# Optimization experiments

Measured on AMD Instinct MI355X. Metric: run time of the kernel, lower is better.

## Reference

```python
import jax, jax.numpy as jnp
import numpy as np
from jax import lax


def setup_inputs() -> dict:
    key = jax.random.key(0)
    x = jax.random.normal(key, (4, 8192, 3), dtype=jnp.float32)
    return {"x": x, "k": 16}


def reference(x, k):
    p = x[..., :3]                                  # (B, N, 3)
    # Brute-force KNN: squared euclidean distances (B, N, N)
    sq = jnp.sum(p * p, axis=-1)                    # (B, N)
    d2 = sq[:, :, None] + sq[:, None, :] - 2.0 * jnp.einsum('bnd,bmd->bnm', p, p)
    _, idx = lax.top_k(-d2, k)                      # (B, N, k), nearest (incl. self)
    # Gather neighbors per batch
    neighbors = jax.vmap(lambda pts, ids: pts[ids])(p, idx)   # (B, N, k, 3)
    mean = jnp.mean(neighbors, axis=2, keepdims=True)          # (B, N, 1, 3)
    diff = neighbors - mean                                    # (B, N, k, 3)
    # cov = mean_k (diff diff^T) over neighbors -> (B, N, 3, 3)
    cov = jnp.einsum('bnki,bnkj->bnij', diff, diff) / k
    ev = jnp.linalg.eigvalsh(cov)                  # ascending: (B, N, 3)
    lambda0 = ev[..., 2]
    lambda1 = ev[..., 1]
    return lambda0 / lambda1
```

## Files before the change

### kernel.cpp

```cpp
#include <hip/hip_runtime.h>
#include <math.h>

#define NB 4
#define NP 8192
#define KK 16
#define QPB 64
#define NPTS (NB * NP)

#define TSAMP 2048
#define TTCH 256
#define BCH 1024
#define NBCH 8
#define CAP 30
#define SROW 34
#define SCH (64 * SROW + 2)
#define K32Q 137
#define J16Q 130
#define PADKEY 0xFFFFFFFFFFFFull
#define TAU_MARGIN 2.5e-4f

#define CSWAP_DESC(a, b) { float _lo = fminf(a, b); float _hi = fmaxf(a, b); a = _hi; b = _lo; }
#define CSWAP_ASC(a, b)  { float _lo = fminf(a, b); float _hi = fmaxf(a, b); a = _lo; b = _hi; }

__device__ __forceinline__ float ref_sq(float x, float y, float z) {
  return __fadd_rn(__fadd_rn(__fmul_rn(x, x), __fmul_rn(y, y)), __fmul_rn(z, z));
}

__device__ __forceinline__ float ref_d2(float qx, float qy, float qz, float sqq,
                                        float cx, float cy, float cz) {
  float sqc = ref_sq(cx, cy, cz);
  float dot = __fadd_rn(__fadd_rn(__fmul_rn(qx, cx), __fmul_rn(qy, cy)),
                        __fmul_rn(qz, cz));
  float s = __fadd_rn(sqq, sqc);
  return __fmaf_rn(-2.0f, dot, s);
}

__device__ __forceinline__ float diff_d2(float qx, float qy, float qz,
                                         float cx, float cy, float cz) {
  float dx = cx - qx, dy = cy - qy, dz = cz - qz;
  return __fmaf_rn(dz, dz, __fmaf_rn(dy, dy, dx * dx));
}

__device__ __forceinline__ unsigned int ord_f32(float d) {
  unsigned int b = __float_as_uint(d);
  return b ^ ((b >> 31) ? 0xFFFFFFFFu : 0x80000000u);
}

__device__ __forceinline__ double eigen_ratio_tail(
    float cxx, float cyy, float czz, float cxy, float cxz, float cyz,
    float k1) {
  double a   = (double)__fmul_rn(cxx, k1), b = (double)__fmul_rn(cyy, k1);
  double c2  = (double)__fmul_rn(czz, k1);
  double dxy = (double)__fmul_rn(cxy, k1), exz = (double)__fmul_rn(cxz, k1);
  double fyz = (double)__fmul_rn(cyz, k1);
  double qm = (a + b + c2) / 3.0;
  double p1 = dxy * dxy + exz * exz + fyz * fyz;
  double aa = a - qm, bb = b - qm, cc = c2 - qm;
  double p2 = aa * aa + bb * bb + cc * cc + 2.0 * p1;
  if (p2 <= 0.0) return 1.0;
  double p  = sqrt(p2 / 6.0);
  double ip = 1.0 / p;
  double b00 = aa * ip, b11 = bb * ip, b22 = cc * ip;
  double b01 = dxy * ip, b02 = exz * ip, b12 = fyz * ip;
  double detB = b00 * (b11 * b22 - b12 * b12)
              - b01 * (b01 * b22 - b12 * b02)
              + b02 * (b01 * b12 - b11 * b02);
  double r = 0.5 * detB;
  r = fmin(1.0, fmax(-1.0, r));
  const double dcl = 2.0 * r;
  float phif = acosf((float)r) * (1.0f / 3.0f);
  double y0 = 2.0 * (double)cosf(phif);
  double y2 = 2.0 * (double)cosf(phif + 2.0943951f);
#pragma unroll
  for (int it = 0; it < 3; ++it) {
    double g0 = 3.0 * (y0 * y0 - 1.0);
    if (fabs(g0) > 1e-4) y0 -= (y0 * y0 * y0 - 3.0 * y0 - dcl) / g0;
    double g2 = 3.0 * (y2 * y2 - 1.0);
    if (fabs(g2) > 1e-4) y2 -= (y2 * y2 * y2 - 3.0 * y2 - dcl) / g2;
  }
  double e0 = qm + p * y0;
  double e2v = qm + p * y2;
  double e1 = 3.0 * qm - e0 - e2v;
  return e0 / e1;
}

__device__ __forceinline__ void topk_update(float bd[KK], float d[8]) {
  CSWAP_DESC(d[0], d[1]) CSWAP_DESC(d[2], d[3]) CSWAP_DESC(d[4], d[5]) CSWAP_DESC(d[6], d[7])
  CSWAP_DESC(d[0], d[2]) CSWAP_DESC(d[1], d[3]) CSWAP_DESC(d[4], d[6]) CSWAP_DESC(d[5], d[7])
  CSWAP_DESC(d[1], d[2]) CSWAP_DESC(d[5], d[6])
  CSWAP_DESC(d[0], d[4]) CSWAP_DESC(d[1], d[5]) CSWAP_DESC(d[2], d[6]) CSWAP_DESC(d[3], d[7])
  CSWAP_DESC(d[2], d[4]) CSWAP_DESC(d[3], d[5])
  CSWAP_DESC(d[1], d[2]) CSWAP_DESC(d[3], d[4]) CSWAP_DESC(d[5], d[6])
#pragma unroll
  for (int i = 0; i < 8; ++i) bd[8 + i] = fminf(bd[8 + i], d[i]);
#pragma unroll
  for (int i = 0; i < 8; ++i)  CSWAP_ASC(bd[i], bd[i + 8])
#pragma unroll
  for (int i = 0; i < 4; ++i)  CSWAP_ASC(bd[i], bd[i + 4])
#pragma unroll
  for (int i = 8; i < 12; ++i) CSWAP_ASC(bd[i], bd[i + 4])
#pragma unroll
  for (int g = 0; g < 4; ++g) {
    CSWAP_ASC(bd[4 * g + 0], bd[4 * g + 2]) CSWAP_ASC(bd[4 * g + 1], bd[4 * g + 3])
    CSWAP_ASC(bd[4 * g + 0], bd[4 * g + 1]) CSWAP_ASC(bd[4 * g + 2], bd[4 * g + 3])
  }
}

__global__ __launch_bounds__(512, 4) void filter_select_kernel(
    const float* __restrict__ x, float* __restrict__ out) {
  extern __shared__ __align__(16) char smem[];
  float4* samp = (float4*)smem;
  float (*s_t)[64][17] = (float (*)[64][17])smem;
  unsigned short* s_idx = (unsigned short*)smem;
  unsigned int* k32 = (unsigned int*)smem;
  unsigned short* j16s = (unsigned short*)(smem + 35072);
  unsigned short* s_cnt = (unsigned short*)(smem + 51712);
  float* s_tau = (float*)(smem + 52736);

  const int tid   = threadIdx.x;
  const int lane  = tid & 63;
  const int w     = __builtin_amdgcn_readfirstlane(tid >> 6);
  const int group = blockIdx.x;
  const int batch = group >> 7;
  const int qbase = (group & 127) * QPB;
  const float* __restrict__ Xb = x + (size_t)batch * NP * 3;

  const float qx = Xb[3 * (qbase + lane) + 0];
  const float qy = Xb[3 * (qbase + lane) + 1];
  const float qz = Xb[3 * (qbase + lane) + 2];

  {
    const float4* X4 = (const float4*)Xb;
#pragma unroll
    for (int r = 0; r < 3; ++r)
      samp[r * 512 + tid] = X4[r * 512 + tid];
  }
  __syncthreads();

  float bdA[KK], bdB[KK];
  {
    const float* sf = (const float*)samp;
#pragma unroll
    for (int t = 0; t < KK; ++t) { bdA[t] = 3.4e38f; bdB[t] = 3.4e38f; }

    const int j0 = w * TTCH;
    for (int jj = 0; jj < TTCH; jj += 16) {
      float dA[8], dB[8];
#pragma unroll
      for (int u = 0; u < 8; ++u) {
        const int j = 3 * (j0 + jj + u);
        dA[u] = diff_d2(qx, qy, qz, sf[j], sf[j + 1], sf[j + 2]);
      }
#pragma unroll
      for (int u = 0; u < 8; ++u) {
        const int j = 3 * (j0 + jj + 8 + u);
        dB[u] = diff_d2(qx, qy, qz, sf[j], sf[j + 1], sf[j + 2]);
      }
      topk_update(bdA, dA);
      topk_update(bdB, dB);
    }
    topk_update(bdA, &bdB[0]);
    topk_update(bdA, &bdB[8]);
  }
  __syncthreads();

#pragma unroll
  for (int t = 0; t < KK; ++t) s_t[w][lane][t] = bdA[t];
  __syncthreads();

  if (w == 0) {
    float md[KK];
#pragma unroll
    for (int t = 0; t < KK; ++t) md[t] = s_t[0][lane][t];
#pragma unroll
    for (int s2 = 1; s2 < NBCH; ++s2) {
      float d[KK];
#pragma unroll
      for (int t = 0; t < KK; ++t) d[t] = s_t[s2][lane][t];
      topk_update(md, &d[0]);
      topk_update(md, &d[8]);
    }
    s_tau[lane] = md[KK - 1];
  }
  __syncthreads();

  {
    const int j0 = w * BCH;
    const float tau = s_tau[lane] + TAU_MARGIN;
    unsigned short* Srow = &s_idx[w * SCH + lane * SROW];
    int cnt = 0;
    for (int jj = 0; jj < BCH; jj += 16) {
      const float4* xp = (const float4*)(Xb + (size_t)(j0 + jj) * 3);
      float4 cv[12];
#pragma unroll
      for (int u = 0; u < 12; ++u) cv[u] = xp[u];
      const float* f = (const float*)cv;
#pragma unroll
      for (int u = 0; u < 16; ++u) {
        float d = diff_d2(qx, qy, qz, f[3 * u], f[3 * u + 1], f[3 * u + 2]);
        if (d <= tau) {
          if (cnt < CAP) Srow[1 + cnt] = (unsigned short)(j0 + jj + u);
          ++cnt;
        }
      }
    }
    s_cnt[w * 64 + lane] = (unsigned short)cnt;
  }
  __syncthreads();

  const int qlq = tid >> 3;
  const int pch = tid & 7;
  unsigned long long slots[KK];
#pragma unroll
  for (int t = 0; t < KK; ++t) slots[t] = PADKEY;
  {
    const float q2x = Xb[3 * (qbase + qlq) + 0];
    const float q2y = Xb[3 * (qbase + qlq) + 1];
    const float q2z = Xb[3 * (qbase + qlq) + 2];
    const float sq2 = ref_sq(q2x, q2y, q2z);
    const unsigned short* row = &s_idx[pch * SCH + qlq * SROW + 1];
    int cnl = (int)s_cnt[pch * 64 + qlq];
    if (cnl > CAP) cnl = CAP;
    for (int e = 0; e < cnl; e += 8) {
      unsigned long long kv[8];
#pragma unroll
      for (int u = 0; u < 8; ++u) {
        const bool ok = (e + u) < cnl;
        const int j = ok ? (int)row[e + u] : 0;
        const float cx = Xb[3 * j], cy = Xb[3 * j + 1], cz = Xb[3 * j + 2];
        const float dd = ref_d2(q2x, q2y, q2z, sq2, cx, cy, cz);
        kv[u] = ok ? ((((unsigned long long)ord_f32(dd)) << 16) |
                      (unsigned int)j)
                   : PADKEY;
      }
#pragma unroll
      for (int u = 0; u < 8; ++u) {
        const unsigned long long k = kv[u];
        if (k < slots[KK - 1]) {
#pragma unroll
          for (int t = KK - 1; t >= 1; --t) {
            unsigned long long lo =
                (slots[t] < k) ? slots[t] : k;
            slots[t] = (slots[t - 1] > lo) ? slots[t - 1] : lo;
          }
          slots[0] = (slots[0] < k) ? slots[0] : k;
        }
      }
    }
  }
  __syncthreads();

#pragma unroll
  for (int t = 0; t < KK; ++t) {
    k32[qlq * K32Q + pch * 17 + t] = (unsigned int)(slots[t] >> 16);
    j16s[qlq * J16Q + pch * 16 + t] = (unsigned short)(slots[t] & 0xFFFFull);
  }
  __syncthreads();

  if (tid < QPB) {
    const int ql = tid;
    const int qg = batch * NP + qbase + ql;
    const float q2x = Xb[3 * (qbase + ql) + 0];
    const float q2y = Xb[3 * (qbase + ql) + 1];
    const float q2z = Xb[3 * (qbase + ql) + 2];
    const float sq2 = ref_sq(q2x, q2y, q2z);

    int total = 0;
    bool fs = false;
#pragma unroll
    for (int p = 0; p < NBCH; ++p) {
      const int c = (int)s_cnt[p * 64 + ql];
      if (c > CAP) fs = true;
      total += c;
    }
    if (total < KK) fs = true;

    int mjr[KK];
    if (!fs) {
      const unsigned int* kq = k32 + ql * K32Q;
      const unsigned short* jq = j16s + ql * J16Q;
      int head[NBCH];
#pragma unroll
      for (int p = 0; p < NBCH; ++p) head[p] = 0;
#pragma unroll
      for (int t = 0; t < KK; ++t) {
        unsigned long long best = PADKEY;
        int bp = 0;
#pragma unroll
        for (int p = 0; p < NBCH; ++p) {
          const int h = head[p];
          const unsigned long long k =
              (h < KK) ? ((((unsigned long long)kq[p * 17 + h]) << 16) |
                          jq[p * 16 + h])
                       : PADKEY;
          if (k < best) { best = k; bp = p; }
        }
        head[bp]++;
        mjr[t] = (int)(best & 0xFFFFull);
      }
    } else {
      float md[KK];
#pragma unroll
      for (int t = 0; t < KK; ++t) { md[t] = 3.4e38f; mjr[t] = 0; }
      for (int j = 0; j < NP; ++j) {
        float d = ref_d2(q2x, q2y, q2z, sq2,
                         Xb[3 * j], Xb[3 * j + 1], Xb[3 * j + 2]);
        if (d < md[KK - 1]) {
          bool c0 = d < md[0];
#pragma unroll
          for (int t = KK - 1; t >= 1; --t) {
            bool cl = d < md[t];
            bool cp = d < md[t - 1];
            float nv = fmaxf(md[t - 1], fminf(md[t], d));
            mjr[t] = cl ? (cp ? mjr[t - 1] : j) : mjr[t];
            md[t] = nv;
          }
          mjr[0] = c0 ? j : mjr[0];
          md[0] = fminf(md[0], d);
        }
      }
    }

    float px[KK], py[KK], pz[KK];
#pragma unroll
    for (int s = 0; s < KK; ++s) {
      px[s] = Xb[3 * mjr[s]];
      py[s] = Xb[3 * mjr[s] + 1];
      pz[s] = Xb[3 * mjr[s] + 2];
    }

    float sx = 0.f, sy = 0.f, sz = 0.f;
#pragma unroll
    for (int s = 0; s < KK; ++s) {
      sx = __fadd_rn(sx, px[s]);
      sy = __fadd_rn(sy, py[s]);
      sz = __fadd_rn(sz, pz[s]);
    }
    const float k1 = 1.0f / KK;
    const float mx = sx * k1, my = sy * k1, mz = sz * k1;

    float cxx = 0.f, cxy = 0.f, cxz = 0.f, cyy = 0.f, cyz = 0.f, czz = 0.f;
#pragma unroll
    for (int s = 0; s < KK; ++s) {
      float dx = __fsub_rn(px[s], mx);
      float dy = __fsub_rn(py[s], my);
      float dz = __fsub_rn(pz[s], mz);
      cxx = __fadd_rn(cxx, __fmul_rn(dx, dx));
      cxy = __fadd_rn(cxy, __fmul_rn(dx, dy));
      cxz = __fadd_rn(cxz, __fmul_rn(dx, dz));
      cyy = __fadd_rn(cyy, __fmul_rn(dy, dy));
      cyz = __fadd_rn(cyz, __fmul_rn(dy, dz));
      czz = __fadd_rn(czz, __fmul_rn(dz, dz));
    }

    out[qg] = (float)eigen_ratio_tail(cxx, cyy, czz, cxy, cxz, cyz, k1);
  }
}

extern "C" void kernel_launch(void* const* d_in, const int* in_sizes, int n_in,
                              void* d_out, int out_size, void* d_ws, size_t ws_size,
                              hipStream_t stream) {
  const float* x = (const float*)d_in[0];
  float* out = (float*)d_out;
  const size_t fs_lds = 52992;
  filter_select_kernel<<<dim3(512), dim3(512), fs_lds, stream>>>(x, out);
}
```

Measured before the change: 185.5 us.

## Merge per-chunk top-k lists via wavefront shuffles and bitonic merge; branchless candidate append

Drops the two barriers and the LDS staging of each chunk's sorted 16-slot keys. The eight lanes serving a query now merge their lists in registers using xor-shuffles and a bitonic half-cleaner network, so the single-thread 8-way merge per query goes away. The candidate filter loop now writes unconditionally to a clamped slot and increments the count branchlessly, which avoids lane divergence. LDS use drops from about 53 KB to 36 KB, which may allow more blocks per CU. The cost is 48 64-bit shuffles per lane and more register pressure.

```diff
diff --git a/kernel.cpp b/kernel.cpp
--- a/kernel.cpp
+++ b/kernel.cpp
@@ -14,13 +14,13 @@
 #define CAP 30
 #define SROW 34
 #define SCH (64 * SROW + 2)
-#define K32Q 137
-#define J16Q 130
 #define PADKEY 0xFFFFFFFFFFFFull
 #define TAU_MARGIN 2.5e-4f
 
 #define CSWAP_DESC(a, b) { float _lo = fminf(a, b); float _hi = fmaxf(a, b); a = _hi; b = _lo; }
 #define CSWAP_ASC(a, b)  { float _lo = fminf(a, b); float _hi = fmaxf(a, b); a = _lo; b = _hi; }
+#define CSWAP_U64(a, b)  { unsigned long long _lo = (a < b) ? a : b; \
+                           unsigned long long _hi = (a < b) ? b : a; a = _lo; b = _hi; }
 
 __device__ __forceinline__ float ref_sq(float x, float y, float z) {
   return __fadd_rn(__fadd_rn(__fmul_rn(x, x), __fmul_rn(y, y)), __fmul_rn(z, z));
@@ -112,10 +112,8 @@
   float4* samp = (float4*)smem;
   float (*s_t)[64][17] = (float (*)[64][17])smem;
   unsigned short* s_idx = (unsigned short*)smem;
-  unsigned int* k32 = (unsigned int*)smem;
-  unsigned short* j16s = (unsigned short*)(smem + 35072);
-  unsigned short* s_cnt = (unsigned short*)(smem + 51712);
-  float* s_tau = (float*)(smem + 52736);
+  unsigned short* s_cnt = (unsigned short*)(smem + 34848);
+  float* s_tau = (float*)(smem + 35872);
 
   const int tid   = threadIdx.x;
   const int lane  = tid & 63;
@@ -197,11 +195,10 @@
       const float* f = (const float*)cv;
 #pragma unroll
       for (int u = 0; u < 16; ++u) {
-        float d = diff_d2(qx, qy, qz, f[3 * u], f[3 * u + 1], f[3 * u + 2]);
-        if (d <= tau) {
-          if (cnt < CAP) Srow[1 + cnt] = (unsigned short)(j0 + jj + u);
-          ++cnt;
-        }
+        const float d = diff_d2(qx, qy, qz, f[3 * u], f[3 * u + 1], f[3 * u + 2]);
+        const int wofs = (cnt < CAP) ? cnt : CAP;
+        Srow[1 + wofs] = (unsigned short)(j0 + jj + u);
+        cnt += (d <= tau) ? 1 : 0;
       }
     }
     s_cnt[w * 64 + lane] = (unsigned short)cnt;
@@ -248,17 +245,35 @@
       }
     }
   }
-  __syncthreads();
-
-#pragma unroll
-  for (int t = 0; t < KK; ++t) {
-    k32[qlq * K32Q + pch * 17 + t] = (unsigned int)(slots[t] >> 16);
-    j16s[qlq * J16Q + pch * 16 + t] = (unsigned short)(slots[t] & 0xFFFFull);
-  }
-  __syncthreads();
-
-  if (tid < QPB) {
-    const int ql = tid;
+
+#pragma unroll
+  for (int m = 1; m <= 4; m <<= 1) {
+    unsigned long long pr[KK];
+#pragma unroll
+    for (int t = 0; t < KK; ++t)
+      pr[t] = (unsigned long long)__shfl_xor((long long)slots[t], m, 64);
+#pragma unroll
+    for (int t = 0; t < KK; ++t) {
+      const unsigned long long b = pr[KK - 1 - t];
+      slots[t] = (slots[t] < b) ? slots[t] : b;
+    }
+#pragma unroll
+    for (int i = 0; i < 8; ++i)  CSWAP_U64(slots[i], slots[i + 8])
+#pragma unroll
+    for (int i = 0; i < 4; ++i)  CSWAP_U64(slots[i], slots[i + 4])
+#pragma unroll
+    for (int i = 8; i < 12; ++i) CSWAP_U64(slots[i], slots[i + 4])
+#pragma unroll
+    for (int g = 0; g < 4; ++g) {
+      CSWAP_U64(slots[4 * g + 0], slots[4 * g + 2])
+      CSWAP_U64(slots[4 * g + 1], slots[4 * g + 3])
+      CSWAP_U64(slots[4 * g + 0], slots[4 * g + 1])
+      CSWAP_U64(slots[4 * g + 2], slots[4 * g + 3])
+    }
+  }
+
+  if (pch == 0) {
+    const int ql = qlq;
     const int qg = batch * NP + qbase + ql;
     const float q2x = Xb[3 * (qbase + ql) + 0];
     const float q2y = Xb[3 * (qbase + ql) + 1];
@@ -277,27 +292,8 @@
 
     int mjr[KK];
     if (!fs) {
-      const unsigned int* kq = k32 + ql * K32Q;
-      const unsigned short* jq = j16s + ql * J16Q;
-      int head[NBCH];
-#pragma unroll
-      for (int p = 0; p < NBCH; ++p) head[p] = 0;
-#pragma unroll
-      for (int t = 0; t < KK; ++t) {
-        unsigned long long best = PADKEY;
-        int bp = 0;
-#pragma unroll
-        for (int p = 0; p < NBCH; ++p) {
-          const int h = head[p];
-          const unsigned long long k =
-              (h < KK) ? ((((unsigned long long)kq[p * 17 + h]) << 16) |
-                          jq[p * 16 + h])
-                       : PADKEY;
-          if (k < best) { best = k; bp = p; }
-        }
-        head[bp]++;
-        mjr[t] = (int)(best & 0xFFFFull);
-      }
+#pragma unroll
+      for (int t = 0; t < KK; ++t) mjr[t] = (int)(slots[t] & 0xFFFFull);
     } else {
       float md[KK];
 #pragma unroll
@@ -362,6 +358,6 @@
                               hipStream_t stream) {
   const float* x = (const float*)d_in[0];
   float* out = (float*)d_out;
-  const size_t fs_lds = 52992;
+  const size_t fs_lds = 36128;
   filter_select_kernel<<<dim3(512), dim3(512), fs_lds, stream>>>(x, out);
 }
```

Measured after the change: 202.3 us. 9.1% more time.
